# Performance work log

Measured on AMD Instinct MI355X. Metric: run time of the kernel, lower is better.

## Reference

```python
import jax, jax.numpy as jnp
import numpy as np

D_MODEL = 1024
H = 16
D_HEAD = D_MODEL // H  # 64
RANK = 32
ALPHA = 1.0


def _lora_linear(x, W, b, dW, dB):
    # merged weight: W + alpha * (dB @ dW), then x @ W_merged.T + b
    Wm = W + ALPHA * (dB @ dW)
    return x @ Wm.T + b


def setup_inputs() -> dict:
    key = jax.random.key(0)
    ks = jax.random.split(key, 20)
    inp = {"x": jax.random.normal(ks[0], (2, 2048, D_MODEL), dtype=jnp.float32)}
    i = 1
    for name in ("q", "k", "v", "o"):
        inp[f"{name}_W"] = jax.random.normal(ks[i], (D_MODEL, D_MODEL), dtype=jnp.float32) * 0.02; i += 1
        inp[f"{name}_b"] = jnp.zeros((D_MODEL,), dtype=jnp.float32)
        inp[f"{name}_dW"] = jax.random.normal(ks[i], (RANK, D_MODEL), dtype=jnp.float32) * 0.01; i += 1
        inp[f"{name}_dB"] = jax.random.normal(ks[i], (D_MODEL, RANK), dtype=jnp.float32) * 0.01; i += 1
    return inp


def reference(x, q_W, q_b, q_dW, q_dB, k_W, k_b, k_dW, k_dB,
              v_W, v_b, v_dW, v_dB, o_W, o_b, o_dW, o_dB):
    b_s, n, _ = x.shape
    # LoRA-merged QKV projections
    q = _lora_linear(x, q_W, q_b, q_dW, q_dB).reshape(b_s, n, H, D_HEAD)
    k = _lora_linear(x, k_W, k_b, k_dW, k_dB).reshape(b_s, n, H, D_HEAD)
    v = _lora_linear(x, v_W, v_b, v_dW, v_dB).reshape(b_s, n, H, D_HEAD)
    scale = 1.0 / np.sqrt(D_HEAD).astype(np.float32)
    # att: [b, h, nq, nk]
    att = jnp.einsum('bqhd,bkhd->bhqk', q, k) * scale
    att = jax.nn.softmax(att, axis=-1)  # dropout = identity (eval mode)
    out = jnp.einsum('bhqk,bkhd->bqhd', att, v).reshape(b_s, n, H * D_HEAD)
    return _lora_linear(out, o_W, o_b, o_dW, o_dB)
```

## Files before the change

### kernel.cpp

```cpp
#include <hip/hip_runtime.h>

typedef unsigned short ushort_t;
typedef unsigned int u32;
typedef __attribute__((ext_vector_type(8))) short short8;
typedef __attribute__((ext_vector_type(4))) float floatx4;
typedef __attribute__((ext_vector_type(16))) float floatx16;
typedef __attribute__((ext_vector_type(2))) unsigned int uintx2;
typedef __attribute__((ext_vector_type(4))) unsigned int uintx4;

typedef const __attribute__((address_space(1))) u32* gptr_t;
typedef __attribute__((address_space(3))) u32* lptr_t;

__device__ __forceinline__ void async_copy16(void* lds, const void* g) {
  __builtin_amdgcn_global_load_lds((gptr_t)g, (lptr_t)lds, 16, 0, 0);
}

__device__ __forceinline__ ushort_t f2bf(float f) {
  u32 u = __float_as_uint(f);
  u += 0x7fffu + ((u >> 16) & 1u);
  return (ushort_t)(u >> 16);
}

__device__ __forceinline__ floatx4 mfma16(short8 a, short8 b, floatx4 c) {
  return __builtin_amdgcn_mfma_f32_16x16x32_bf16(a, b, c, 0, 0, 0);
}

__device__ __forceinline__ floatx16 mfma32(short8 a, short8 b, floatx16 c) {
  return __builtin_amdgcn_mfma_f32_32x32x16_bf16(a, b, c, 0, 0, 0);
}

__device__ __forceinline__ u32 cvt_pk_bf16(float lo, float hi) {
  u32 r;
  asm("v_cvt_pk_bf16_f32 %0, %1, %2" : "=v"(r) : "v"(lo), "v"(hi));
  return r;
}

__device__ __forceinline__ short8 mkfrag(u32 x0, u32 x1, u32 x2, u32 x3) {
  uintx2 ra = __builtin_amdgcn_permlane32_swap(x0, x2, false, false);
  uintx2 rb = __builtin_amdgcn_permlane32_swap(x1, x3, false, false);
  union { uintx4 u; short8 s; } t;
  t.u[0] = ra[0]; t.u[1] = rb[0]; t.u[2] = ra[1]; t.u[3] = rb[1];
  return t.s;
}

struct alignas(16) F4 { float a, b, c, d; };
struct alignas(8) U4 { ushort_t a, b, c, d; };

#define QSCALE 0.18033688011112043f

__global__ __launch_bounds__(256) void prep_kernel(
    const float* __restrict__ x, ushort_t* __restrict__ xs,
    const float* __restrict__ W0, const float* __restrict__ dW0, const float* __restrict__ dB0,
    const float* __restrict__ W1, const float* __restrict__ dW1, const float* __restrict__ dB1,
    const float* __restrict__ W2, const float* __restrict__ dW2, const float* __restrict__ dB2,
    const float* __restrict__ W3, const float* __restrict__ dW3, const float* __restrict__ dB3,
    ushort_t* __restrict__ Wm) {
  const int bid = blockIdx.x;
  if (bid < 4096) {
    int i = bid * 256 + threadIdx.x;
    F4 v = ((const F4*)x)[i];
    U4 hh = {f2bf(v.a), f2bf(v.b), f2bf(v.c), f2bf(v.d)};
    ((U4*)xs)[i] = hh;
    return;
  }
  const int t = bid - 4096;
  const int layer = t >> 7, sub = t & 127;
  const float* W = (layer == 0) ? W0 : (layer == 1) ? W1 : (layer == 2) ? W2 : W3;
  const float* dW = (layer == 0) ? dW0 : (layer == 1) ? dW1 : (layer == 2) ? dW2 : dW3;
  const float* dB = (layer == 0) ? dB0 : (layer == 1) ? dB1 : (layer == 2) ? dB2 : dB3;
  ushort_t* Wh = Wm + (size_t)layer * 1024 * 1024;
  const int ot = sub * 8;
  const int d0 = threadIdx.x * 4;
  float acc[8][4] = {};
  for (int r = 0; r < 32; ++r) {
    F4 w = *(const F4*)&dW[r * 1024 + d0];
    float wv[4] = {w.a, w.b, w.c, w.d};
#pragma unroll
    for (int o = 0; o < 8; ++o) {
      float s = dB[(ot + o) * 32 + r];
#pragma unroll
      for (int j = 0; j < 4; ++j) acc[o][j] += s * wv[j];
    }
  }
#pragma unroll
  for (int o = 0; o < 8; ++o) {
    F4 w = *(const F4*)&W[(ot + o) * 1024 + d0];
    U4 hh = {f2bf(w.a + acc[o][0]), f2bf(w.b + acc[o][1]),
             f2bf(w.c + acc[o][2]), f2bf(w.d + acc[o][3])};
    *(U4*)&Wh[(ot + o) * 1024 + d0] = hh;
  }
}

template <int MODE, int TN>
__global__ __launch_bounds__(256) void gemm_bt(
    const ushort_t* __restrict__ A, const ushort_t* __restrict__ B,
    const float* __restrict__ b0, const float* __restrict__ b1,
    const float* __restrict__ b2,
    ushort_t* __restrict__ C, ushort_t* __restrict__ vth,
    float* __restrict__ Cf, const int M, const int N, const int K) {
  constexpr int NT2 = TN / 32;
  __shared__ __align__(16) ushort_t lA[2][128 * 32], lB[2][TN * 32];
  const int tid = threadIdx.x;
  const int wave = tid >> 6, lane = tid & 63;
  const int lo4 = lane & 15, quad = lane >> 4;
  const int n0 = blockIdx.x * TN, m0 = blockIdx.y * 128;
  const int wm = (wave >> 1) * 64, wn = (wave & 1) * (TN / 2);

  floatx4 acc[4][NT2];
  const floatx4 zero4 = {0.f, 0.f, 0.f, 0.f};
#pragma unroll
  for (int mt = 0; mt < 4; ++mt)
#pragma unroll
    for (int nt = 0; nt < NT2; ++nt) acc[mt][nt] = zero4;

  const int strow = lane >> 2;
  const int stcol = (lane & 3) * 8;

  const int NTILES = K >> 5;
  {
#pragma unroll
    for (int i = 0; i < 2; ++i) {
      const int g = wave * 2 + i;
      async_copy16(&lA[0][g * 512], A + (size_t)(m0 + g * 16 + strow) * K + stcol);
    }
#pragma unroll
    for (int i = 0; i < TN / 64; ++i) {
      const int g = wave * (TN / 64) + i;
      async_copy16(&lB[0][g * 512], B + (size_t)(n0 + g * 16 + strow) * K + stcol);
    }
  }
  __syncthreads();

  for (int t = 0; t < NTILES; ++t) {
    const int cur = t & 1;
    if (t + 1 < NTILES) {
      const int kk = (t + 1) << 5;
#pragma unroll
      for (int i = 0; i < 2; ++i) {
        const int g = wave * 2 + i;
        async_copy16(&lA[cur ^ 1][g * 512], A + (size_t)(m0 + g * 16 + strow) * K + kk + stcol);
      }
#pragma unroll
      for (int i = 0; i < TN / 64; ++i) {
        const int g = wave * (TN / 64) + i;
        async_copy16(&lB[cur ^ 1][g * 512], B + (size_t)(n0 + g * 16 + strow) * K + kk + stcol);
      }
    }
    short8 a_[4], b_[NT2];
#pragma unroll
    for (int t2 = 0; t2 < 4; ++t2)
      a_[t2] = *(const short8*)&lA[cur][(wm + t2 * 16 + lo4) * 32 + quad * 8];
#pragma unroll
    for (int t2 = 0; t2 < NT2; ++t2)
      b_[t2] = *(const short8*)&lB[cur][(wn + t2 * 16 + lo4) * 32 + quad * 8];
#pragma unroll
    for (int mt = 0; mt < 4; ++mt)
#pragma unroll
      for (int nt = 0; nt < NT2; ++nt)
        acc[mt][nt] = (MODE == 0) ? mfma16(a_[mt], b_[nt], acc[mt][nt])
                                  : mfma16(b_[nt], a_[mt], acc[mt][nt]);
    if (t + 1 < NTILES) __syncthreads();
  }

  if (MODE == 0) {
#pragma unroll
    for (int nt = 0; nt < NT2; ++nt) {
      const int col = n0 + wn + nt * 16 + lo4;
      const float bias =
          (col < 1024) ? b0[col] : (col < 2048) ? b1[col - 1024] : b2[col - 2048];
      if (col < 2048) {
#pragma unroll
        for (int mt = 0; mt < 4; ++mt)
#pragma unroll
          for (int r = 0; r < 4; ++r) {
            const int row = m0 + wm + mt * 16 + quad * 4 + r;
            float c = acc[mt][nt][r] + bias;
            if (col < 1024) c *= QSCALE;
            C[(size_t)row * 2048 + col] = f2bf(c);
          }
      } else {
        const int d = col - 2048;
#pragma unroll
        for (int mt = 0; mt < 4; ++mt) {
          const int rowb = m0 + wm + mt * 16 + quad * 4;
          const size_t vrow = (size_t)(((rowb >> 11) * 16 + (d >> 6)) * 64 + (d & 63));
          U4 hh = {f2bf(acc[mt][nt][0] + bias), f2bf(acc[mt][nt][1] + bias),
                   f2bf(acc[mt][nt][2] + bias), f2bf(acc[mt][nt][3] + bias)};
          *(U4*)&vth[vrow * 2048 + (rowb & 2047)] = hh;
        }
      }
    }
  } else {
#pragma unroll
    for (int nt = 0; nt < NT2; ++nt) {
      const int col0 = n0 + wn + nt * 16 + quad * 4;
      const F4 bv = *(const F4*)&b0[col0];
#pragma unroll
      for (int mt = 0; mt < 4; ++mt) {
        const int row = m0 + wm + mt * 16 + lo4;
        F4 o = {acc[mt][nt][0] + bv.a, acc[mt][nt][1] + bv.b,
                acc[mt][nt][2] + bv.c, acc[mt][nt][3] + bv.d};
        *(F4*)&Cf[(size_t)row * N + col0] = o;
      }
    }
  }
}

__global__ __launch_bounds__(512, 4) void attn_kernel(
    const ushort_t* __restrict__ qk, const ushort_t* __restrict__ vt,
    ushort_t* __restrict__ at) {
  __shared__ __align__(16) ushort_t Kh[2][2][64 * 64];
  __shared__ __align__(16) ushort_t Vh[2][2][64 * 64];
  const int bid = blockIdx.x;
  const int xcd = bid & 7, g = bid >> 3;
  const int bh = xcd * 4 + (g >> 4), qt = g & 15;
  const int b = bh >> 4, h = bh & 15;
  const int tid = threadIdx.x;
  const int wave = tid >> 6, lane = tid & 63;
  const int rowg = wave & 3, half = wave >> 2;
  const int l31 = lane & 31, hi = lane >> 5, l7 = lane & 7;
  const int hi8 = hi * 8;

  short8 qf[4];
  {
    const ushort_t* gq =
        qk + (size_t)(b * 2048 + qt * 128 + rowg * 32 + l31) * 2048 + h * 64 + hi8;
#pragma unroll
    for (int st = 0; st < 4; ++st) qf[st] = *(const short8*)(gq + st * 16);
  }

  floatx16 O[2], Lacc;
#pragma unroll
  for (int i = 0; i < 16; ++i) { O[0][i] = 0.f; O[1][i] = 0.f; Lacc[i] = 0.f; }

  short8 onesf;
  {
    union { uintx4 u; short8 s; } ou;
    ou.u[0] = 0x3F803F80u; ou.u[1] = 0x3F803F80u;
    ou.u[2] = 0x3F803F80u; ou.u[3] = 0x3F803F80u;
    onesf = ou.s;
  }

  const int stile = wave >> 1, spart = wave & 1;
  const int strow = lane >> 3;
  const int stswz = (l7 ^ strow) * 8;
  const ushort_t* Ksrc = qk + (size_t)b * 2048 * 2048 + 1024 + h * 64;
  const ushort_t* Vsrc = vt + (size_t)bh * 64 * 2048;

#define STAGE(buf, t_)                                                             \
  {                                                                                \
    const int kt_ = 2 * (t_) + (stile & 1);                                        \
    if (stile < 2) {                                                               \
      const ushort_t* s_ =                                                         \
          Ksrc + (size_t)(kt_ * 64 + spart * 32 + strow) * 2048 + stswz;           \
      ushort_t* d_ = &Kh[buf][stile & 1][spart * 32 * 64];                         \
      _Pragma("unroll") for (int i_ = 0; i_ < 4; ++i_)                             \
          async_copy16(d_ + i_ * 512, s_ + (size_t)i_ * 8 * 2048);                 \
    } else {                                                                       \
      const ushort_t* s_ =                                                         \
          Vsrc + (size_t)(spart * 32 + strow) * 2048 + kt_ * 64 + stswz;           \
      ushort_t* d_ = &Vh[buf][stile & 1][spart * 32 * 64];                         \
      _Pragma("unroll") for (int i_ = 0; i_ < 4; ++i_)                             \
          async_copy16(d_ + i_ * 512, s_ + (size_t)i_ * 8 * 2048);                 \
    }                                                                              \
  }

  STAGE(0, 0);
  __syncthreads();

  for (int t = 0; t < 16; ++t) {
    const int cur = t & 1;
    if (t + 1 < 16) STAGE(cur ^ 1, t + 1);

    floatx16 s0, s1;
#pragma unroll
    for (int i = 0; i < 16; ++i) { s0[i] = 0.f; s1[i] = 0.f; }
    __builtin_amdgcn_s_setprio(1);
#pragma unroll
    for (int st = 0; st < 4; ++st) {
      const int c = ((st * 2 + hi) ^ l7) * 8;
      s0 = mfma32(*(const short8*)&Kh[cur][half][l31 * 64 + c], qf[st], s0);
      s1 = mfma32(*(const short8*)&Kh[cur][half][(32 + l31) * 64 + c], qf[st], s1);
    }
    __builtin_amdgcn_s_setprio(0);

    u32 a0[8], a1[8];
#pragma unroll
    for (int j = 0; j < 8; ++j) {
      a0[j] = cvt_pk_bf16(__builtin_amdgcn_exp2f(s0[2 * j]),
                          __builtin_amdgcn_exp2f(s0[2 * j + 1]));
      a1[j] = cvt_pk_bf16(__builtin_amdgcn_exp2f(s1[2 * j]),
                          __builtin_amdgcn_exp2f(s1[2 * j + 1]));
    }

    short8 pb00 = mkfrag(a0[0], a0[1], a0[2], a0[3]);
    short8 pb01 = mkfrag(a0[4], a0[5], a0[6], a0[7]);
    short8 pb10 = mkfrag(a1[0], a1[1], a1[2], a1[3]);
    short8 pb11 = mkfrag(a1[4], a1[5], a1[6], a1[7]);

    __builtin_amdgcn_s_setprio(1);
    Lacc = mfma32(onesf, pb00, Lacc);
    Lacc = mfma32(onesf, pb01, Lacc);
    Lacc = mfma32(onesf, pb10, Lacc);
    Lacc = mfma32(onesf, pb11, Lacc);
#pragma unroll
    for (int dblk = 0; dblk < 2; ++dblk) {
      const int vr = (dblk * 32 + l31) * 64;
      O[dblk] = mfma32(*(const short8*)&Vh[cur][half][vr + ((0 + hi) ^ l7) * 8], pb00, O[dblk]);
      O[dblk] = mfma32(*(const short8*)&Vh[cur][half][vr + ((2 + hi) ^ l7) * 8], pb01, O[dblk]);
      O[dblk] = mfma32(*(const short8*)&Vh[cur][half][vr + ((4 + hi) ^ l7) * 8], pb10, O[dblk]);
      O[dblk] = mfma32(*(const short8*)&Vh[cur][half][vr + ((6 + hi) ^ l7) * 8], pb11, O[dblk]);
    }
    __builtin_amdgcn_s_setprio(0);
    if (t + 1 < 16) __syncthreads();
  }
#undef STAGE

  float l = Lacc[0];

  float* Pf0 = (float*)&Kh[0][0][0];
  float* Pf1 = (float*)&Vh[0][0][0];
  __syncthreads();
  if (half == 1) {
    const int base = rowg * 1280 + lane * 20;
#pragma unroll
    for (int j = 0; j < 16; ++j) Pf0[base + j] = O[0][j];
#pragma unroll
    for (int j = 0; j < 16; ++j) Pf1[base + j] = O[1][j];
    Pf0[base + 16] = l;
  }
  __syncthreads();
  if (half == 0) {
    const int base = rowg * 1280 + lane * 20;
#pragma unroll
    for (int j = 0; j < 16; ++j) O[0][j] += Pf0[base + j];
#pragma unroll
    for (int j = 0; j < 16; ++j) O[1][j] += Pf1[base + j];
    l += Pf0[base + 16];
    const float linv = 1.f / l;
    ushort_t* out =
        at + (size_t)(b * 2048 + qt * 128 + rowg * 32 + l31) * 1024 + h * 64;
#pragma unroll
    for (int dblk = 0; dblk < 2; ++dblk)
#pragma unroll
      for (int gr = 0; gr < 4; ++gr) {
        U4 hh = {f2bf(O[dblk][4 * gr + 0] * linv), f2bf(O[dblk][4 * gr + 1] * linv),
                 f2bf(O[dblk][4 * gr + 2] * linv), f2bf(O[dblk][4 * gr + 3] * linv)};
        *(U4*)&out[dblk * 32 + gr * 8 + hi * 4] = hh;
      }
  }
}

extern "C" void kernel_launch(void* const* d_in, const int* in_sizes, int n_in,
                              void* d_out, int out_size, void* d_ws, size_t ws_size,
                              hipStream_t stream) {
  const float* x = (const float*)d_in[0];
  const float* qW = (const float*)d_in[1];
  const float* qb = (const float*)d_in[2];
  const float* qdW = (const float*)d_in[3];
  const float* qdB = (const float*)d_in[4];
  const float* kW = (const float*)d_in[5];
  const float* kb = (const float*)d_in[6];
  const float* kdW = (const float*)d_in[7];
  const float* kdB = (const float*)d_in[8];
  const float* vW = (const float*)d_in[9];
  const float* vb = (const float*)d_in[10];
  const float* vdW = (const float*)d_in[11];
  const float* vdB = (const float*)d_in[12];
  const float* oW = (const float*)d_in[13];
  const float* ob = (const float*)d_in[14];
  const float* odW = (const float*)d_in[15];
  const float* odB = (const float*)d_in[16];

  char* ws = (char*)d_ws;
  const size_t MB = 1024u * 1024u;
  const size_t WELEM = 1024u * 1024u;
  ushort_t* xs = (ushort_t*)(ws + 0 * MB);
  ushort_t* Wm = (ushort_t*)(ws + 8 * MB);
  ushort_t* qk = (ushort_t*)(ws + 16 * MB);
  ushort_t* vt = (ushort_t*)(ws + 32 * MB);
  ushort_t* at = xs;

  prep_kernel<<<4608, 256, 0, stream>>>(x, xs, qW, qdW, qdB, kW, kdW, kdB,
                                        vW, vdW, vdB, oW, odW, odB, Wm);
  gemm_bt<0, 128><<<dim3(24, 32), 256, 0, stream>>>(xs, Wm, qb, kb, vb,
                                                    qk, vt, nullptr, 4096, 3072, 1024);
  attn_kernel<<<512, 512, 0, stream>>>(qk, vt, at);
  gemm_bt<1, 64><<<dim3(16, 32), 256, 0, stream>>>(at, Wm + 3 * WELEM, ob, nullptr,
                                                   nullptr, nullptr, nullptr,
                                                   (float*)d_out, 4096, 1024, 1024);
}
```

Before: 216.9 us.

## Software-pipeline attention loop: overlap QK of next tile with PV of previous

New measurement: 462.5 us. 113% more time.

```diff
diff --git a/kernel.cpp b/kernel.cpp
--- a/kernel.cpp
+++ b/kernel.cpp
@@ -210,7 +210,7 @@
     const ushort_t* __restrict__ qk, const ushort_t* __restrict__ vt,
     ushort_t* __restrict__ at) {
   __shared__ __align__(16) ushort_t Kh[2][2][64 * 64];
-  __shared__ __align__(16) ushort_t Vh[2][2][64 * 64];
+  __shared__ __align__(16) ushort_t Vh[3][2][64 * 64];
   const int bid = blockIdx.x;
   const int xcd = bid & 7, g = bid >> 3;
   const int bh = xcd * 4 + (g >> 4), qt = g & 15;
@@ -229,17 +229,11 @@
     for (int st = 0; st < 4; ++st) qf[st] = *(const short8*)(gq + st * 16);
   }
 
-  floatx16 O[2], Lacc;
-#pragma unroll
-  for (int i = 0; i < 16; ++i) { O[0][i] = 0.f; O[1][i] = 0.f; Lacc[i] = 0.f; }
-
-  short8 onesf;
-  {
-    union { uintx4 u; short8 s; } ou;
-    ou.u[0] = 0x3F803F80u; ou.u[1] = 0x3F803F80u;
-    ou.u[2] = 0x3F803F80u; ou.u[3] = 0x3F803F80u;
-    onesf = ou.s;
-  }
+  floatx16 O[2], zero16;
+#pragma unroll
+  for (int i = 0; i < 16; ++i) { O[0][i] = 0.f; O[1][i] = 0.f; zero16[i] = 0.f; }
+  float l_acc[4] = {0.f, 0.f, 0.f, 0.f};
+  u32 pa0[8], pa1[8];
 
   const int stile = wave >> 1, spart = wave & 1;
   const int strow = lane >> 3;
@@ -247,76 +241,97 @@
   const ushort_t* Ksrc = qk + (size_t)b * 2048 * 2048 + 1024 + h * 64;
   const ushort_t* Vsrc = vt + (size_t)bh * 64 * 2048;
 
-#define STAGE(buf, t_)                                                             \
+#define STAGE(kb_, vb_, t_)                                                        \
   {                                                                                \
     const int kt_ = 2 * (t_) + (stile & 1);                                        \
     if (stile < 2) {                                                               \
       const ushort_t* s_ =                                                         \
           Ksrc + (size_t)(kt_ * 64 + spart * 32 + strow) * 2048 + stswz;           \
-      ushort_t* d_ = &Kh[buf][stile & 1][spart * 32 * 64];                         \
+      ushort_t* d_ = &Kh[kb_][stile & 1][spart * 32 * 64];                         \
       _Pragma("unroll") for (int i_ = 0; i_ < 4; ++i_)                             \
           async_copy16(d_ + i_ * 512, s_ + (size_t)i_ * 8 * 2048);                 \
     } else {                                                                       \
       const ushort_t* s_ =                                                         \
           Vsrc + (size_t)(spart * 32 + strow) * 2048 + kt_ * 64 + stswz;           \
-      ushort_t* d_ = &Vh[buf][stile & 1][spart * 32 * 64];                         \
+      ushort_t* d_ = &Vh[vb_][stile & 1][spart * 32 * 64];                         \
       _Pragma("unroll") for (int i_ = 0; i_ < 4; ++i_)                             \
           async_copy16(d_ + i_ * 512, s_ + (size_t)i_ * 8 * 2048);                 \
     }                                                                              \
   }
 
-  STAGE(0, 0);
+#define QKBLK(kb_, s0_, s1_)                                                       \
+  {                                                                                \
+    const ushort_t* kb = &Kh[kb_][half][0];                                        \
+    __builtin_amdgcn_s_setprio(1);                                                 \
+    s0_ = mfma32(*(const short8*)&kb[l31 * 64 + ((0 + hi) ^ l7) * 8], qf[0], zero16); \
+    s1_ = mfma32(*(const short8*)&kb[(32 + l31) * 64 + ((0 + hi) ^ l7) * 8], qf[0],   \
+                 zero16);                                                          \
+    _Pragma("unroll") for (int st = 1; st < 4; ++st) {                             \
+      const int c = ((st * 2 + hi) ^ l7) * 8;                                      \
+      s0_ = mfma32(*(const short8*)&kb[l31 * 64 + c], qf[st], s0_);                \
+      s1_ = mfma32(*(const short8*)&kb[(32 + l31) * 64 + c], qf[st], s1_);         \
+    }                                                                              \
+    __builtin_amdgcn_s_setprio(0);                                                 \
+  }
+
+#define PVBLK(vb_)                                                                 \
+  {                                                                                \
+    short8 pb00 = mkfrag(pa0[0], pa0[1], pa0[2], pa0[3]);                          \
+    short8 pb01 = mkfrag(pa0[4], pa0[5], pa0[6], pa0[7]);                          \
+    short8 pb10 = mkfrag(pa1[0], pa1[1], pa1[2], pa1[3]);                          \
+    short8 pb11 = mkfrag(pa1[4], pa1[5], pa1[6], pa1[7]);                          \
+    const ushort_t* vb = &Vh[vb_][half][0];                                        \
+    __builtin_amdgcn_s_setprio(1);                                                 \
+    _Pragma("unroll") for (int dblk = 0; dblk < 2; ++dblk) {                       \
+      const int vr = (dblk * 32 + l31) * 64;                                       \
+      O[dblk] = mfma32(*(const short8*)&vb[vr + ((0 + hi) ^ l7) * 8], pb00, O[dblk]); \
+      O[dblk] = mfma32(*(const short8*)&vb[vr + ((2 + hi) ^ l7) * 8], pb01, O[dblk]); \
+      O[dblk] = mfma32(*(const short8*)&vb[vr + ((4 + hi) ^ l7) * 8], pb10, O[dblk]); \
+      O[dblk] = mfma32(*(const short8*)&vb[vr + ((6 + hi) ^ l7) * 8], pb11, O[dblk]); \
+    }                                                                              \
+    __builtin_amdgcn_s_setprio(0);                                                 \
+  }
+
+#define PACK(s0_, s1_)                                                             \
+  {                                                                                \
+    _Pragma("unroll") for (int j = 0; j < 8; ++j) {                                \
+      float p0a = __builtin_amdgcn_exp2f(s0_[2 * j]);                              \
+      float p0b = __builtin_amdgcn_exp2f(s0_[2 * j + 1]);                          \
+      float p1a = __builtin_amdgcn_exp2f(s1_[2 * j]);                              \
+      float p1b = __builtin_amdgcn_exp2f(s1_[2 * j + 1]);                          \
+      l_acc[j & 3] += (p0a + p0b) + (p1a + p1b);                                   \
+      pa0[j] = cvt_pk_bf16(p0a, p0b);                                              \
+      pa1[j] = cvt_pk_bf16(p1a, p1b);                                              \
+    }                                                                              \
+  }
+
+  STAGE(0, 0, 0);
   __syncthreads();
-
-  for (int t = 0; t < 16; ++t) {
-    const int cur = t & 1;
-    if (t + 1 < 16) STAGE(cur ^ 1, t + 1);
-
+  STAGE(1, 1, 1);
+  {
     floatx16 s0, s1;
-#pragma unroll
-    for (int i = 0; i < 16; ++i) { s0[i] = 0.f; s1[i] = 0.f; }
-    __builtin_amdgcn_s_setprio(1);
-#pragma unroll
-    for (int st = 0; st < 4; ++st) {
-      const int c = ((st * 2 + hi) ^ l7) * 8;
-      s0 = mfma32(*(const short8*)&Kh[cur][half][l31 * 64 + c], qf[st], s0);
-      s1 = mfma32(*(const short8*)&Kh[cur][half][(32 + l31) * 64 + c], qf[st], s1);
-    }
-    __builtin_amdgcn_s_setprio(0);
-
-    u32 a0[8], a1[8];
-#pragma unroll
-    for (int j = 0; j < 8; ++j) {
-      a0[j] = cvt_pk_bf16(__builtin_amdgcn_exp2f(s0[2 * j]),
-                          __builtin_amdgcn_exp2f(s0[2 * j + 1]));
-      a1[j] = cvt_pk_bf16(__builtin_amdgcn_exp2f(s1[2 * j]),
-                          __builtin_amdgcn_exp2f(s1[2 * j + 1]));
-    }
-
-    short8 pb00 = mkfrag(a0[0], a0[1], a0[2], a0[3]);
-    short8 pb01 = mkfrag(a0[4], a0[5], a0[6], a0[7]);
-    short8 pb10 = mkfrag(a1[0], a1[1], a1[2], a1[3]);
-    short8 pb11 = mkfrag(a1[4], a1[5], a1[6], a1[7]);
-
-    __builtin_amdgcn_s_setprio(1);
-    Lacc = mfma32(onesf, pb00, Lacc);
-    Lacc = mfma32(onesf, pb01, Lacc);
-    Lacc = mfma32(onesf, pb10, Lacc);
-    Lacc = mfma32(onesf, pb11, Lacc);
-#pragma unroll
-    for (int dblk = 0; dblk < 2; ++dblk) {
-      const int vr = (dblk * 32 + l31) * 64;
-      O[dblk] = mfma32(*(const short8*)&Vh[cur][half][vr + ((0 + hi) ^ l7) * 8], pb00, O[dblk]);
-      O[dblk] = mfma32(*(const short8*)&Vh[cur][half][vr + ((2 + hi) ^ l7) * 8], pb01, O[dblk]);
-      O[dblk] = mfma32(*(const short8*)&Vh[cur][half][vr + ((4 + hi) ^ l7) * 8], pb10, O[dblk]);
-      O[dblk] = mfma32(*(const short8*)&Vh[cur][half][vr + ((6 + hi) ^ l7) * 8], pb11, O[dblk]);
-    }
-    __builtin_amdgcn_s_setprio(0);
-    if (t + 1 < 16) __syncthreads();
-  }
+    QKBLK(0, s0, s1);
+    PACK(s0, s1);
+  }
+  __syncthreads();
+
+#pragma unroll
+  for (int t = 1; t < 16; ++t) {
+    if (t < 15) STAGE((t + 1) & 1, (t + 1) % 3, t + 1);
+    floatx16 s0, s1;
+    QKBLK(t & 1, s0, s1);
+    PVBLK((t - 1) % 3);
+    PACK(s0, s1);
+    if (t < 15) __syncthreads();
+  }
+  PVBLK(15 % 3);
 #undef STAGE
-
-  float l = Lacc[0];
+#undef QKBLK
+#undef PVBLK
+#undef PACK
+
+  float l = (l_acc[0] + l_acc[1]) + (l_acc[2] + l_acc[3]);
+  l += __shfl_xor(l, 32);
 
   float* Pf0 = (float*)&Kh[0][0][0];
   float* Pf1 = (float*)&Vh[0][0][0];
```
